# Kernel optimization log

Hardware: AMD Instinct MI355X
Metric: run time of the kernel (lower is better)

The kernel has to match this reference:

```python
import jax, jax.numpy as jnp
import numpy as np

B, D_IN, H, OUT = 4096, 2048, 4096, 1000
TEMPERATURE = 0.5


def _l2_normalize(w):
    return w / jnp.linalg.norm(w, axis=1, keepdims=True)


def setup_inputs() -> dict:
    key = jax.random.key(0)
    ks = jax.random.split(key, 8)
    x = jax.random.normal(ks[0], (B, D_IN), dtype=jnp.float32)
    kohonen_weights = _l2_normalize(jax.random.normal(ks[1], (H, D_IN), dtype=jnp.float32))
    # MLP: 4096 -> 2048 -> 1024 -> 1000 (hidden_layers=2, div=2)
    def lin(k, fan_in, fan_out):
        kw, kb = jax.random.split(k)
        bound = 1.0 / np.sqrt(fan_in)
        W = jax.random.uniform(kw, (fan_out, fan_in), minval=-bound, maxval=bound, dtype=jnp.float32)
        b = jax.random.uniform(kb, (fan_out,), minval=-bound, maxval=bound, dtype=jnp.float32)
        return W, b
    w1, b1 = lin(ks[2], H, H // 2)
    w2, b2 = lin(ks[3], H // 2, H // 4)
    w3, b3 = lin(ks[4], H // 4, OUT)
    return {"x": x, "kohonen_weights": kohonen_weights,
            "w1": w1, "b1": b1, "w2": w2, "b2": b2, "w3": w3, "b3": b3}


def reference(x, kohonen_weights, w1, b1, w2, b2, w3, b3):
    # pairwise euclidean distances [B, H] via expanded GEMM (cdist p=2)
    x2 = jnp.sum(x * x, axis=1, keepdims=True)            # [B,1]
    w2sq = jnp.sum(kohonen_weights * kohonen_weights, axis=1)  # [H]
    d2 = x2 + w2sq[None, :] - 2.0 * (x @ kohonen_weights.T)
    distances = jnp.sqrt(jnp.maximum(d2, 1e-12))
    winners = jnp.argmin(distances, axis=1)
    soft = jax.nn.softmax(-distances / TEMPERATURE, axis=1)
    # MLP (dropout=0 / eval mode)
    h = jax.nn.relu(soft @ w1.T + b1)
    h = jax.nn.relu(h @ w2.T + b2)
    output = h @ w3.T + b3
    return output, winners
```

## Files before the change

### kernel.cpp

```cpp
#include <hip/hip_runtime.h>
#include <hip/hip_bf16.h>
#include <stdint.h>

typedef __attribute__((ext_vector_type(4))) float f32x4;
typedef __attribute__((ext_vector_type(8))) __bf16 bf16x8;
typedef unsigned short u16;
typedef unsigned long long u64;

__device__ __forceinline__ u16 f2bf(float f){
  unsigned u = __float_as_uint(f);
  u += 0x7fffu + ((u >> 16) & 1u);
  return (u16)(u >> 16);
}
__device__ __forceinline__ float bf2f(u16 v){
  return __uint_as_float(((unsigned)v) << 16);
}

__device__ __forceinline__ void gload16(const u16* g, u16* l){
  __builtin_amdgcn_global_load_lds(
      (__attribute__((address_space(1))) void*)g,
      (__attribute__((address_space(3))) void*)l, 16, 0, 0);
}

template<int N> __device__ __forceinline__ void waitcnt_vm(){
  if constexpr (N==0) asm volatile("s_waitcnt vmcnt(0)" ::: "memory");
  else if constexpr (N==4) asm volatile("s_waitcnt vmcnt(4)" ::: "memory");
  else if constexpr (N==8) asm volatile("s_waitcnt vmcnt(8)" ::: "memory");
}

__global__ __launch_bounds__(64)
void cvt_rows(const float* __restrict__ src, u16* __restrict__ dst,
              float* __restrict__ sq)
{
#pragma clang fp contract(off)
  const int row = blockIdx.x;
  const int l = threadIdx.x;
  const float* r = src + (size_t)row * 2048;
  const f32x4* r4 = (const f32x4*)r;
  ushort4* d4 = (ushort4*)(dst + (size_t)row * 2048);
#pragma unroll
  for (int i = 0; i < 8; i++){
    f32x4 v = r4[l + 64*i];
    ushort4 o;
    o.x = f2bf(v.x); o.y = f2bf(v.y); o.z = f2bf(v.z); o.w = f2bf(v.w);
    d4[l + 64*i] = o;
  }
  float leaf = 0.f;
  if (l < 16){
    const f32x4* p4 = (const f32x4*)(r + l*128);
    f32x4 a0 = {0.f,0.f,0.f,0.f}, a1 = {0.f,0.f,0.f,0.f};
#pragma unroll
    for (int i = 0; i < 32; i += 2){
      f32x4 v0 = p4[i], v1 = p4[i+1];
      a0 = a0 + v0*v0;
      a1 = a1 + v1*v1;
    }
    leaf = ((a0.x+a0.y)+(a0.z+a0.w))+((a1.x+a1.y)+(a1.z+a1.w));
  }
#pragma unroll
  for (int s = 1; s < 16; s <<= 1){
    float o = __shfl_down(leaf, s);
    if ((l & (2*s - 1)) == 0) leaf = leaf + o;
  }
  if (l == 0) sq[row] = leaf;
}

__global__ __launch_bounds__(256)
void cvt_mat(const float* __restrict__ src, u16* __restrict__ dst, int n4)
{
  const f32x4* s4 = (const f32x4*)src;
  ushort4* d4 = (ushort4*)dst;
  for (int i = blockIdx.x*256 + threadIdx.x; i < n4; i += gridDim.x*256){
    f32x4 v = s4[i];
    ushort4 o;
    o.x = f2bf(v.x); o.y = f2bf(v.y); o.z = f2bf(v.z); o.w = f2bf(v.w);
    d4[i] = o;
  }
}

__global__ __launch_bounds__(512, 2)
void gemm8p(const u16* __restrict__ A, int lda,
            const u16* __restrict__ Bm, int ldb,
            u16* __restrict__ Cb, int N, int Kpp, int nbn, int blkpp)
{
  constexpr int BUFB = 65536;
  extern __shared__ char lds[];
  const int t = threadIdx.x;
  const int nwg = gridDim.x;
  const int cpx = nwg >> 3;
  const int bid = blockIdx.x;
  const int wg  = (bid & 7)*cpx + (bid >> 3);
  const int piece = wg / blkpp;
  const int rem = wg % blkpp;
  const int bm = rem / nbn, bn = rem % nbn;
  const int brow = bm*256, bcol = bn*256;
  const u16* Ab = A + (size_t)brow*lda + (size_t)piece*Kpp;
  const u16* Bb = Bm + (size_t)bcol*ldb + (size_t)piece*Kpp;
  u16* Cp = Cb + (size_t)piece * 4096 * N;

  const int l = t & 63, w = t >> 6;
  const int wm = w >> 2, wn = w & 3;
  const int wr = wm*128, wc = wn*64;
  const int fr = l & 15, fq = l >> 4;
  const int cb0 = (fq ^ (fr & 7)) << 4;
  const int cb1 = ((4 + fq) ^ (fr & 7)) << 4;
  const int scol8 = ((t & 7) ^ ((t >> 3) & 7)) * 8;
  const int srow = t >> 3;

  const int nt = Kpp >> 6;
  f32x4 acc[8][4] = {};

  auto stage_half = [&](int kt, int h){
    const int nb = kt & 1;
    const u16* src = (h < 2) ? Ab : Bb;
    const int ld = (h < 2) ? lda : ldb;
    const u16* s0 = src + (size_t)((h & 1)*128 + srow)*ld + kt*64 + scol8;
    char* d = lds + nb*BUFB + (h >> 1)*32768 + (h & 1)*16384 + t*16;
    gload16(s0, (u16*)d);
    gload16(s0 + (size_t)64*ld, (u16*)(d + 8192));
  };
  auto ldA = [&](int buf, int m, int cb)->bf16x8 {
    return *(const bf16x8*)(lds + buf*BUFB + (wr + m*16 + fr)*128 + cb);
  };
  auto ldB = [&](int buf, int n, int cb)->bf16x8 {
    return *(const bf16x8*)(lds + buf*BUFB + 32768 + (wc + n*16 + fr)*128 + cb);
  };

  stage_half(0,0); stage_half(0,1); stage_half(0,2); stage_half(0,3);
  stage_half(1,0); stage_half(1,1);
  waitcnt_vm<4>();
  __builtin_amdgcn_s_barrier();

  for (int kt = 0; kt < nt; kt++){
    const int buf = kt & 1;
    bf16x8 av0[8], av1[8], bv0[4], bv1[4];

#pragma unroll
    for (int m = 0; m < 8; m++) av0[m] = ldA(buf, m, cb0);
#pragma unroll
    for (int n = 0; n < 4; n++) bv0[n] = ldB(buf, n, cb0);
    if (kt + 1 < nt) stage_half(kt + 1, 2);
    __builtin_amdgcn_s_setprio(1);
#pragma unroll
    for (int m = 0; m < 8; m++)
#pragma unroll
      for (int n = 0; n < 4; n++)
        acc[m][n] = __builtin_amdgcn_mfma_f32_16x16x32_bf16(av0[m], bv0[n], acc[m][n], 0, 0, 0);
    __builtin_amdgcn_s_setprio(0);
#pragma unroll
    for (int m = 0; m < 8; m++) av1[m] = ldA(buf, m, cb1);
    if (kt + 1 < nt) stage_half(kt + 1, 3);
    asm volatile("s_waitcnt lgkmcnt(0)" ::: "memory");
    __builtin_amdgcn_s_barrier();

#pragma unroll
    for (int n = 0; n < 4; n++) bv1[n] = ldB(buf, n, cb1);
    if (kt + 2 < nt) stage_half(kt + 2, 0);
    __builtin_amdgcn_s_setprio(1);
#pragma unroll
    for (int m = 0; m < 4; m++)
#pragma unroll
      for (int n = 0; n < 4; n++)
        acc[m][n] = __builtin_amdgcn_mfma_f32_16x16x32_bf16(av1[m], bv1[n], acc[m][n], 0, 0, 0);
    __builtin_amdgcn_s_setprio(0);
    if (kt + 2 < nt) stage_half(kt + 2, 1);
    __builtin_amdgcn_s_setprio(1);
#pragma unroll
    for (int m = 4; m < 8; m++)
#pragma unroll
      for (int n = 0; n < 4; n++)
        acc[m][n] = __builtin_amdgcn_mfma_f32_16x16x32_bf16(av1[m], bv1[n], acc[m][n], 0, 0, 0);
    __builtin_amdgcn_s_setprio(0);

    if (kt + 1 < nt){
      if (kt <= nt - 3) waitcnt_vm<4>();
      else              waitcnt_vm<0>();
      __builtin_amdgcn_s_barrier();
    }
  }

  __builtin_amdgcn_s_barrier();
  u16* ep = (u16*)(lds + w*16384);
#pragma unroll
  for (int m = 0; m < 8; m++)
#pragma unroll
    for (int n = 0; n < 4; n++)
#pragma unroll
      for (int r = 0; r < 4; r++)
        ep[(m*16 + fq*4 + r)*64 + n*16 + fr] = f2bf(acc[m][n][r]);
  asm volatile("s_waitcnt lgkmcnt(0)" ::: "memory");
  const int erow = l >> 3, ecb = (l & 7)*16;
#pragma unroll
  for (int it = 0; it < 16; it++){
    const int row = it*8 + erow;
    f32x4 v = *(const f32x4*)((const char*)ep + row*128 + ecb);
    char* gp = (char*)Cp + (((size_t)(brow + wr + row))*N + (bcol + wc))*2 + ecb;
    *(f32x4*)gp = v;
  }
}

__global__ __launch_bounds__(256)
void combine_relu(const u16* __restrict__ p0, const u16* __restrict__ p1,
                  const float* __restrict__ bias, u16* __restrict__ out)
{
  const int n4 = 4096*2048/4;
  for (int i = blockIdx.x*256 + threadIdx.x; i < n4; i += gridDim.x*256){
    ushort4 a = ((const ushort4*)p0)[i];
    ushort4 b = ((const ushort4*)p1)[i];
    const int col = (i*4) & 2047;
    f32x4 bi = *(const f32x4*)(bias + col);
    ushort4 o;
    o.x = f2bf(fmaxf(bf2f(a.x) + bf2f(b.x) + bi.x, 0.f));
    o.y = f2bf(fmaxf(bf2f(a.y) + bf2f(b.y) + bi.y, 0.f));
    o.z = f2bf(fmaxf(bf2f(a.z) + bf2f(b.z) + bi.z, 0.f));
    o.w = f2bf(fmaxf(bf2f(a.w) + bf2f(b.w) + bi.w, 0.f));
    ((ushort4*)out)[i] = o;
  }
}

template<int BM, int BN, int WM, int WN, int EPI, int MINW>
__global__ __launch_bounds__(WM*WN*64, MINW)
void gemm_p(const u16* __restrict__ A, const u16* __restrict__ Bm,
            float* __restrict__ Cf, u16* __restrict__ Cb,
            const float* __restrict__ bias,
            int M, int N, int K, int ncols, int nbn)
{
  constexpr int T  = WM*WN*64;
  constexpr int FM = BM/(WM*16);
  constexpr int FN = BN/(WN*16);
  constexpr int ABYTES = BM*64;
  constexpr int BUFB   = (BM+BN)*64;
  constexpr int RA = ABYTES/(T*16);
  constexpr int RB = (BN*64)/(T*16);
  constexpr int IF = RA + RB;
  extern __shared__ char lds[];

  const int t = threadIdx.x;
  const int nwg = gridDim.x;
  const int cpx = nwg >> 3;
  const int bid = blockIdx.x;
  const int wg  = (bid & 7)*cpx + (bid >> 3);
  const int bm = wg / nbn, bn = wg % nbn;
  const int brow = bm*BM, bcol = bn*BN;

  const int l = t & 63, w = t >> 6;
  const int wm = w / WN, wn = w % WN;
  const int wr = wm*(FM*16), wc = wn*(FN*16);
  const int fr = l & 15, fq = l >> 4, fk = fq*8;
  const int xk = fk ^ (((fr >> 1) & 3) << 3);

  const int srow = t >> 2;
  const int scol = ((t & 3)*8) ^ (((t >> 3) & 3) << 3);

  const u16* agp[RA]; const u16* bgp[RB];
#pragma unroll
  for (int r = 0; r < RA; r++)
    agp[r] = A + (size_t)(brow + r*(T>>2) + srow)*K + scol;
#pragma unroll
  for (int r = 0; r < RB; r++)
    bgp[r] = Bm + (size_t)(bcol + r*(T>>2) + srow)*K + scol;

  f32x4 acc[FM][FN] = {};
  const int nt = K >> 5;

  auto stageA = [&](int kt, int buf){
    char* dst = lds + buf*BUFB + t*16;
#pragma unroll
    for (int r = 0; r < RA; r++)
      gload16(agp[r] + (kt << 5), (u16*)(dst + r*T*16));
  };
  auto stageB = [&](int kt, int buf){
    char* dst = lds + buf*BUFB + ABYTES + t*16;
#pragma unroll
    for (int r = 0; r < RB; r++)
      gload16(bgp[r] + (kt << 5), (u16*)(dst + r*T*16));
  };

  stageA(0, 0); stageB(0, 0);
  stageA(1, 1); stageB(1, 1);
  stageA(2, 2); stageB(2, 2);
  waitcnt_vm<8>();
  __builtin_amdgcn_s_barrier();

  for (int kt = 0; kt < nt; kt++){
    const int buf = kt & 3;
    const u16* As = (const u16*)(lds + buf*BUFB);
    const u16* Bs = (const u16*)(lds + buf*BUFB + ABYTES);
    const bool pre = (kt + 3 < nt);
    const int nbuf = (kt + 3) & 3;

    bf16x8 av[FM], bv[FN];
#pragma unroll
    for (int m = 0; m < FM; m++)
      av[m] = *(const bf16x8*)(As + (wr + m*16 + fr)*32 + xk);
#pragma unroll
    for (int n = 0; n < FN; n++)
      bv[n] = *(const bf16x8*)(Bs + (wc + n*16 + fr)*32 + xk);
    if (pre){ stageA(kt + 3, nbuf); stageB(kt + 3, nbuf); }
    __builtin_amdgcn_s_setprio(1);
#pragma unroll
    for (int m = 0; m < FM; m++)
#pragma unroll
      for (int n = 0; n < FN; n++)
        acc[m][n] = __builtin_amdgcn_mfma_f32_16x16x32_bf16(av[m], bv[n], acc[m][n], 0, 0, 0);
    __builtin_amdgcn_s_setprio(0);

    if (kt + 1 < nt){
      if (kt + 3 < nt)      waitcnt_vm<8>();
      else if (kt + 2 < nt) waitcnt_vm<4>();
      else                  waitcnt_vm<0>();
      __builtin_amdgcn_s_barrier();
    }
  }

  __builtin_amdgcn_s_barrier();
  if (EPI == 1){
    u16* ep = (u16*)(lds + w*8192);
#pragma unroll
    for (int n = 0; n < FN; n++){
      const float bvv = bias[bcol + wc + n*16 + fr];
#pragma unroll
      for (int m = 0; m < FM; m++)
#pragma unroll
        for (int r = 0; r < 4; r++)
          ep[(m*16 + fq*4 + r)*64 + n*16 + fr] = f2bf(fmaxf(acc[m][n][r] + bvv, 0.f));
    }
    asm volatile("s_waitcnt lgkmcnt(0)" ::: "memory");
    const int erow = l >> 3, ecb = (l & 7)*16;
#pragma unroll
    for (int it = 0; it < 8; it++){
      const int row = it*8 + erow;
      f32x4 v = *(const f32x4*)((const char*)ep + row*128 + ecb);
      char* gp = (char*)Cb + (((size_t)(brow + wr + row))*N + (bcol + wc))*2 + ecb;
      *(f32x4*)gp = v;
    }
  } else {
    float* ep = (float*)(lds + w*16384);
#pragma unroll
    for (int n = 0; n < FN; n++){
      const int gcol = bcol + wc + n*16 + fr;
      const float bvv = (gcol < ncols) ? bias[gcol] : 0.f;
#pragma unroll
      for (int m = 0; m < FM; m++)
#pragma unroll
        for (int r = 0; r < 4; r++)
          ep[(m*16 + fq*4 + r)*64 + n*16 + fr] = acc[m][n][r] + bvv;
    }
    asm volatile("s_waitcnt lgkmcnt(0)" ::: "memory");
    const int erow = l >> 4, ecb = (l & 15)*16;
    const int gcol0 = bcol + wc + (l & 15)*4;
#pragma unroll
    for (int it = 0; it < 16; it++){
      const int row = it*4 + erow;
      f32x4 v = *(const f32x4*)((const char*)ep + row*256 + ecb);
      if (gcol0 < ncols)
        *(f32x4*)(Cf + (size_t)(brow + wr + row)*ncols + gcol0) = v;
    }
  }
}

__global__ __launch_bounds__(256)
void row_softmax(const u16* __restrict__ Sb, const float* __restrict__ x2,
                 const float* __restrict__ w2sq,
                 const float* __restrict__ x, const float* __restrict__ W,
                 u16* __restrict__ soft, float* __restrict__ winners)
{
  const int b = blockIdx.x, t = threadIdx.x;
  const float x2b = x2[b];
  const ushort4* S4 = (const ushort4*)(Sb + (size_t)b*4096);
  const f32x4* W24 = (const f32x4*)w2sq;
  float dv[16];
  float bd = 3.0e38f; int bc = 0;
#pragma unroll
  for (int i = 0; i < 4; i++){
    ushort4 s = S4[t + 256*i];
    f32x4 wv = W24[t + 256*i];
    float sf[4] = {bf2f(s.x), bf2f(s.y), bf2f(s.z), bf2f(s.w)};
#pragma unroll
    for (int j = 0; j < 4; j++){
      float u = x2b + wv[j];
      float d2 = u - 2.0f*sf[j];
      float d = __fsqrt_rn(fmaxf(d2, 1e-12f));
      dv[i*4 + j] = d;
      if (d < bd){ bd = d; bc = (t + 256*i)*4 + j; }
    }
  }
  u64 key = ((u64)__float_as_uint(bd) << 32) | (unsigned)bc;
#pragma unroll
  for (int s = 1; s < 64; s <<= 1){
    u64 o = __shfl_xor(key, s);
    if (o < key) key = o;
  }
  __shared__ u64 wk[4];
  __shared__ double csum[4];
  __shared__ float fred[4];
  __shared__ int ccnt;
  __shared__ int cand[32];
  if ((t & 63) == 0) wk[t >> 6] = key;
  if (t == 0) ccnt = 0;
  __syncthreads();
  u64 k0 = wk[0];
  if (wk[1] < k0) k0 = wk[1];
  if (wk[2] < k0) k0 = wk[2];
  if (wk[3] < k0) k0 = wk[3];
  const float dmin = __uint_as_float((unsigned)(k0 >> 32));

  const float thr = dmin + 0.01f;
#pragma unroll
  for (int i = 0; i < 4; i++)
#pragma unroll
    for (int j = 0; j < 4; j++)
      if (dv[i*4 + j] <= thr){
        int p = atomicAdd(&ccnt, 1);
        if (p < 32) cand[p] = (t + 256*i)*4 + j;
      }
  __syncthreads();
  const int nc = min(ccnt, 32);

  float bestd = 3.0e38f; int besti = 0x7fffffff;
  const f32x4* xp = (const f32x4*)(x + (size_t)b*2048) + t*2;
  f32x4 xv0 = xp[0], xv1 = xp[1];
  for (int c = 0; c < nc; c++){
    const int h = cand[c];
    const f32x4* wp = (const f32x4*)(W + (size_t)h*2048) + t*2;
    f32x4 wv0 = wp[0], wv1 = wp[1];
    double a = 0.0;
#pragma unroll
    for (int j = 0; j < 4; j++) a += (double)xv0[j]*(double)wv0[j];
#pragma unroll
    for (int j = 0; j < 4; j++) a += (double)xv1[j]*(double)wv1[j];
#pragma unroll
    for (int s = 1; s < 64; s <<= 1) a += __shfl_xor(a, s);
    if ((t & 63) == 0) csum[t >> 6] = a;
    __syncthreads();
    if (t == 0){
      double tt = (csum[0] + csum[1]) + (csum[2] + csum[3]);
      float t32 = (float)tt;
      float u = x2b + w2sq[h];
      float d2 = u - 2.0f*t32;
      float d = __fsqrt_rn(fmaxf(d2, 1e-12f));
      if (d < bestd || (d == bestd && h < besti)){ bestd = d; besti = h; }
    }
    __syncthreads();
  }
  if (t == 0) winners[b] = (float)besti;

  float es = 0.f;
#pragma unroll
  for (int i = 0; i < 16; i++) es += __expf(-2.0f*(dv[i] - dmin));
#pragma unroll
  for (int s = 1; s < 64; s <<= 1) es += __shfl_xor(es, s);
  if ((t & 63) == 0) fred[t >> 6] = es;
  __syncthreads();
  const float tot = (fred[0] + fred[1]) + (fred[2] + fred[3]);
  const float inv = 1.0f / tot;
  ushort4* o4 = (ushort4*)(soft + (size_t)b*4096);
#pragma unroll
  for (int i = 0; i < 4; i++){
    ushort4 o;
    o.x = f2bf(__expf(-2.0f*(dv[i*4+0] - dmin))*inv);
    o.y = f2bf(__expf(-2.0f*(dv[i*4+1] - dmin))*inv);
    o.z = f2bf(__expf(-2.0f*(dv[i*4+2] - dmin))*inv);
    o.w = f2bf(__expf(-2.0f*(dv[i*4+3] - dmin))*inv);
    o4[t + 256*i] = o;
  }
}

extern "C" void kernel_launch(void* const* d_in, const int* in_sizes, int n_in,
                              void* d_out, int out_size, void* d_ws, size_t ws_size,
                              hipStream_t stream)
{
  const float* x  = (const float*)d_in[0];
  const float* Wk = (const float*)d_in[1];
  const float* w1 = (const float*)d_in[2];
  const float* b1 = (const float*)d_in[3];
  const float* w2 = (const float*)d_in[4];
  const float* b2 = (const float*)d_in[5];
  const float* w3 = (const float*)d_in[6];
  const float* b3 = (const float*)d_in[7];
  float* out = (float*)d_out;
  float* winners = out + (size_t)4096*1000;

  char* ws = (char*)d_ws;
  const size_t MB = 1u << 20;
  u16* Sb    = (u16*)(ws);
  u16* soft  = (u16*)(ws + 32*MB);
  u16* w1b   = (u16*)(ws + 64*MB);
  u16* w2b   = (u16*)(ws + 80*MB);
  u16* w3b   = (u16*)(ws + 84*MB);
  float* x2  = (float*)(ws + 86*MB);
  float* w2s = x2 + 4096;
  u16* xb    = (u16*)(ws + 88*MB);
  u16* wb    = (u16*)(ws + 104*MB);
  u16* P0    = (u16*)(ws + 88*MB);
  u16* P1    = (u16*)(ws + 104*MB);
  u16* h1    = (u16*)(ws);
  u16* h2    = (u16*)(ws + 16*MB);

  cvt_rows<<<4096, 64, 0, stream>>>(x, xb, x2);
  cvt_rows<<<4096, 64, 0, stream>>>(Wk, wb, w2s);
  cvt_mat<<<2048, 256, 0, stream>>>(w1, w1b, 2048*4096/4);
  cvt_mat<<<1024, 256, 0, stream>>>(w2, w2b, 1024*2048/4);
  hipMemsetAsync(w3b, 0, (size_t)1024*1024*2, stream);
  cvt_mat<<<512, 256, 0, stream>>>(w3, w3b, 1000*1024/4);

  hipFuncSetAttribute((const void*)gemm8p,
                      hipFuncAttributeMaxDynamicSharedMemorySize, 131072);

  gemm8p<<<256, 512, 131072, stream>>>(xb, 2048, wb, 2048, Sb,
                                       4096, 2048, 16, 256);

  row_softmax<<<4096, 256, 0, stream>>>(Sb, x2, w2s, x, Wk, soft, winners);

  gemm8p<<<256, 512, 131072, stream>>>(soft, 4096, w1b, 4096, P0,
                                       2048, 2048, 8, 128);
  combine_relu<<<2048, 256, 0, stream>>>(P0, P1, b1, h1);

  hipFuncSetAttribute((const void*)gemm_p<128,128,2,2,1,3>,
                      hipFuncAttributeMaxDynamicSharedMemorySize, 4*256*64);
  gemm_p<128,128,2,2,1,3><<<256, 256, 4*256*64, stream>>>(
      h1, w2b, nullptr, h2, b2, 4096, 1024, 2048, 0, 8);

  hipFuncSetAttribute((const void*)gemm_p<128,128,2,2,2,3>,
                      hipFuncAttributeMaxDynamicSharedMemorySize, 4*256*64);
  gemm_p<128,128,2,2,2,3><<<256, 256, 4*256*64, stream>>>(
      h2, w3b, out, nullptr, b3, 4096, 1024, 1024, 1000, 8);
}
```

Baseline: 259.1 us.

## Replace 256x256 GEMM with 256x128 tile, 3-stage K-32 pipeline

Swaps the 512-thread, 256x256-tile, double-buffered K=64 GEMM for a 256-thread kernel using 256x128 tiles and a triple-buffered K=32 LDS pipeline with a simpler single-phase loop. The grid doubles to 512 workgroups and LDS drops to 72KB, with an epilogue row padding added to cut bank conflicts. The aim is more workgroups per CU and deeper prefetch to hide global-load latency. The cost is more barriers per unit of K and less reuse per tile, since the B panel is narrower and each K step is shorter.

Result: slower. 282.8 us (+9.1%).

```diff
diff --git a/kernel.cpp b/kernel.cpp
--- a/kernel.cpp
+++ b/kernel.cpp
@@ -23,9 +23,11 @@
 }
 
 template<int N> __device__ __forceinline__ void waitcnt_vm(){
-  if constexpr (N==0) asm volatile("s_waitcnt vmcnt(0)" ::: "memory");
-  else if constexpr (N==4) asm volatile("s_waitcnt vmcnt(4)" ::: "memory");
-  else if constexpr (N==8) asm volatile("s_waitcnt vmcnt(8)" ::: "memory");
+  if constexpr (N==0)  asm volatile("s_waitcnt vmcnt(0)" ::: "memory");
+  else if constexpr (N==4)  asm volatile("s_waitcnt vmcnt(4)" ::: "memory");
+  else if constexpr (N==6)  asm volatile("s_waitcnt vmcnt(6)" ::: "memory");
+  else if constexpr (N==8)  asm volatile("s_waitcnt vmcnt(8)" ::: "memory");
+  else if constexpr (N==12) asm volatile("s_waitcnt vmcnt(12)" ::: "memory");
 }
 
 __global__ __launch_bounds__(64)
@@ -78,12 +80,13 @@
   }
 }
 
-__global__ __launch_bounds__(512, 2)
-void gemm8p(const u16* __restrict__ A, int lda,
-            const u16* __restrict__ Bm, int ldb,
-            u16* __restrict__ Cb, int N, int Kpp, int nbn, int blkpp)
-{
-  constexpr int BUFB = 65536;
+__global__ __launch_bounds__(256, 2)
+void gemmA(const u16* __restrict__ A, int lda,
+           const u16* __restrict__ Bm, int ldb,
+           u16* __restrict__ Cb, int N, int Kpp, int nbn, int blkpp)
+{
+  constexpr int BUFB = 24576;
+  constexpr int ABYTES = 16384;
   extern __shared__ char lds[];
   const int t = threadIdx.x;
   const int nwg = gridDim.x;
@@ -93,107 +96,90 @@
   const int piece = wg / blkpp;
   const int rem = wg % blkpp;
   const int bm = rem / nbn, bn = rem % nbn;
-  const int brow = bm*256, bcol = bn*256;
+  const int brow = bm*256, bcol = bn*128;
   const u16* Ab = A + (size_t)brow*lda + (size_t)piece*Kpp;
   const u16* Bb = Bm + (size_t)bcol*ldb + (size_t)piece*Kpp;
   u16* Cp = Cb + (size_t)piece * 4096 * N;
 
   const int l = t & 63, w = t >> 6;
-  const int wm = w >> 2, wn = w & 3;
+  const int wm = w >> 1, wn = w & 1;
   const int wr = wm*128, wc = wn*64;
   const int fr = l & 15, fq = l >> 4;
-  const int cb0 = (fq ^ (fr & 7)) << 4;
-  const int cb1 = ((4 + fq) ^ (fr & 7)) << 4;
-  const int scol8 = ((t & 7) ^ ((t >> 3) & 7)) * 8;
-  const int srow = t >> 3;
-
-  const int nt = Kpp >> 6;
+  const int xk = (fq ^ ((fr >> 1) & 3))*8;
+
+  const int srow = t >> 2;
+  const int scol = ((t & 3) ^ ((t >> 3) & 3))*8;
+
+  const u16* agp[4]; const u16* bgp[2];
+#pragma unroll
+  for (int r = 0; r < 4; r++)
+    agp[r] = Ab + (size_t)(r*64 + srow)*lda + scol;
+#pragma unroll
+  for (int r = 0; r < 2; r++)
+    bgp[r] = Bb + (size_t)(r*64 + srow)*ldb + scol;
+
   f32x4 acc[8][4] = {};
-
-  auto stage_half = [&](int kt, int h){
-    const int nb = kt & 1;
-    const u16* src = (h < 2) ? Ab : Bb;
-    const int ld = (h < 2) ? lda : ldb;
-    const u16* s0 = src + (size_t)((h & 1)*128 + srow)*ld + kt*64 + scol8;
-    char* d = lds + nb*BUFB + (h >> 1)*32768 + (h & 1)*16384 + t*16;
-    gload16(s0, (u16*)d);
-    gload16(s0 + (size_t)64*ld, (u16*)(d + 8192));
+  const int nt = Kpp >> 5;
+
+  auto stage = [&](int kt, int buf){
+    char* dst = lds + buf*BUFB + t*16;
+#pragma unroll
+    for (int r = 0; r < 4; r++)
+      gload16(agp[r] + (kt << 5), (u16*)(dst + r*4096));
+#pragma unroll
+    for (int r = 0; r < 2; r++)
+      gload16(bgp[r] + (kt << 5), (u16*)(dst + ABYTES + r*4096));
   };
-  auto ldA = [&](int buf, int m, int cb)->bf16x8 {
-    return *(const bf16x8*)(lds + buf*BUFB + (wr + m*16 + fr)*128 + cb);
-  };
-  auto ldB = [&](int buf, int n, int cb)->bf16x8 {
-    return *(const bf16x8*)(lds + buf*BUFB + 32768 + (wc + n*16 + fr)*128 + cb);
-  };
-
-  stage_half(0,0); stage_half(0,1); stage_half(0,2); stage_half(0,3);
-  stage_half(1,0); stage_half(1,1);
-  waitcnt_vm<4>();
+
+  stage(0, 0); stage(1, 1); stage(2, 2);
+  waitcnt_vm<12>();
   __builtin_amdgcn_s_barrier();
 
+  int buf = 0;
   for (int kt = 0; kt < nt; kt++){
-    const int buf = kt & 1;
-    bf16x8 av0[8], av1[8], bv0[4], bv1[4];
-
-#pragma unroll
-    for (int m = 0; m < 8; m++) av0[m] = ldA(buf, m, cb0);
-#pragma unroll
-    for (int n = 0; n < 4; n++) bv0[n] = ldB(buf, n, cb0);
-    if (kt + 1 < nt) stage_half(kt + 1, 2);
+    const u16* As = (const u16*)(lds + buf*BUFB);
+    const u16* Bs = (const u16*)(lds + buf*BUFB + ABYTES);
+    const int nbuf = (buf + 2 < 3) ? buf + 2 : buf - 1;
+
+    bf16x8 av[8], bv[4];
+#pragma unroll
+    for (int m = 0; m < 8; m++)
+      av[m] = *(const bf16x8*)(As + (wr + m*16 + fr)*32 + xk);
+#pragma unroll
+    for (int n = 0; n < 4; n++)
+      bv[n] = *(const bf16x8*)(Bs + (wc + n*16 + fr)*32 + xk);
+    if (kt + 2 < nt) stage(kt + 2, nbuf);
     __builtin_amdgcn_s_setprio(1);
 #pragma unroll
     for (int m = 0; m < 8; m++)
 #pragma unroll
       for (int n = 0; n < 4; n++)
-        acc[m][n] = __builtin_amdgcn_mfma_f32_16x16x32_bf16(av0[m], bv0[n], acc[m][n], 0, 0, 0);
+        acc[m][n] = __builtin_amdgcn_mfma_f32_16x16x32_bf16(av[m], bv[n], acc[m][n], 0, 0, 0);
     __builtin_amdgcn_s_setprio(0);
-#pragma unroll
-    for (int m = 0; m < 8; m++) av1[m] = ldA(buf, m, cb1);
-    if (kt + 1 < nt) stage_half(kt + 1, 3);
-    asm volatile("s_waitcnt lgkmcnt(0)" ::: "memory");
-    __builtin_amdgcn_s_barrier();
-
-#pragma unroll
-    for (int n = 0; n < 4; n++) bv1[n] = ldB(buf, n, cb1);
-    if (kt + 2 < nt) stage_half(kt + 2, 0);
-    __builtin_amdgcn_s_setprio(1);
-#pragma unroll
-    for (int m = 0; m < 4; m++)
-#pragma unroll
-      for (int n = 0; n < 4; n++)
-        acc[m][n] = __builtin_amdgcn_mfma_f32_16x16x32_bf16(av1[m], bv1[n], acc[m][n], 0, 0, 0);
-    __builtin_amdgcn_s_setprio(0);
-    if (kt + 2 < nt) stage_half(kt + 2, 1);
-    __builtin_amdgcn_s_setprio(1);
-#pragma unroll
-    for (int m = 4; m < 8; m++)
-#pragma unroll
-      for (int n = 0; n < 4; n++)
-        acc[m][n] = __builtin_amdgcn_mfma_f32_16x16x32_bf16(av1[m], bv1[n], acc[m][n], 0, 0, 0);
-    __builtin_amdgcn_s_setprio(0);
 
     if (kt + 1 < nt){
-      if (kt <= nt - 3) waitcnt_vm<4>();
-      else              waitcnt_vm<0>();
+      if (kt + 2 < nt) waitcnt_vm<6>();
+      else             waitcnt_vm<0>();
       __builtin_amdgcn_s_barrier();
     }
+    buf = (buf + 1 < 3) ? buf + 1 : 0;
   }
 
   __builtin_amdgcn_s_barrier();
-  u16* ep = (u16*)(lds + w*16384);
+  u16* ep = (u16*)(lds + w*17408);
 #pragma unroll
   for (int m = 0; m < 8; m++)
 #pragma unroll
     for (int n = 0; n < 4; n++)
 #pragma unroll
       for (int r = 0; r < 4; r++)
-        ep[(m*16 + fq*4 + r)*64 + n*16 + fr] = f2bf(acc[m][n][r]);
+        ep[(m*16 + fq*4 + r)*68 + n*16 + fr] = f2bf(acc[m][n][r]);
   asm volatile("s_waitcnt lgkmcnt(0)" ::: "memory");
   const int erow = l >> 3, ecb = (l & 7)*16;
 #pragma unroll
   for (int it = 0; it < 16; it++){
     const int row = it*8 + erow;
-    f32x4 v = *(const f32x4*)((const char*)ep + row*128 + ecb);
+    f32x4 v = *(const f32x4*)((const char*)ep + row*136 + ecb);
     char* gp = (char*)Cp + (((size_t)(brow + wr + row))*N + (bcol + wc))*2 + ecb;
     *(f32x4*)gp = v;
   }
@@ -232,7 +218,6 @@
   constexpr int BUFB   = (BM+BN)*64;
   constexpr int RA = ABYTES/(T*16);
   constexpr int RB = (BN*64)/(T*16);
-  constexpr int IF = RA + RB;
   extern __shared__ char lds[];
 
   const int t = threadIdx.x;
@@ -504,16 +489,16 @@
   hipMemsetAsync(w3b, 0, (size_t)1024*1024*2, stream);
   cvt_mat<<<512, 256, 0, stream>>>(w3, w3b, 1000*1024/4);
 
-  hipFuncSetAttribute((const void*)gemm8p,
-                      hipFuncAttributeMaxDynamicSharedMemorySize, 131072);
-
-  gemm8p<<<256, 512, 131072, stream>>>(xb, 2048, wb, 2048, Sb,
-                                       4096, 2048, 16, 256);
+  hipFuncSetAttribute((const void*)gemmA,
+                      hipFuncAttributeMaxDynamicSharedMemorySize, 73728);
+
+  gemmA<<<512, 256, 73728, stream>>>(xb, 2048, wb, 2048, Sb,
+                                     4096, 2048, 32, 512);
 
   row_softmax<<<4096, 256, 0, stream>>>(Sb, x2, w2s, x, Wk, soft, winners);
 
-  gemm8p<<<256, 512, 131072, stream>>>(soft, 4096, w1b, 4096, P0,
-                                       2048, 2048, 8, 128);
+  gemmA<<<512, 256, 73728, stream>>>(soft, 4096, w1b, 4096, P0,
+                                     2048, 2048, 16, 256);
   combine_relu<<<2048, 256, 0, stream>>>(P0, P1, b1, h1);
 
   hipFuncSetAttribute((const void*)gemm_p<128,128,2,2,1,3>,
```

## Triple-buffer A tiles in big GEMM and fuse conversion kernels

Applied to the files above, without the earlier changes.

The 256x256 GEMM now uses 160KB of LDS: the A operand gets a three-deep ring buffer and B a double buffer. This removes the mid-iteration barrier and lets A prefetch run two tiles ahead. The epilogue LDS staging rows are padded to 68 elements to cut bank conflicts. The six input-conversion launches and the memset are merged into two kernels, with w3 zero padding done inline. The larger LDS footprint limits occupancy to one workgroup per CU.

New measurement: 251.0 us. 3.1% less time.

```diff
diff --git a/kernel.cpp b/kernel.cpp
--- a/kernel.cpp
+++ b/kernel.cpp
@@ -23,17 +23,22 @@
 }
 
 template<int N> __device__ __forceinline__ void waitcnt_vm(){
-  if constexpr (N==0) asm volatile("s_waitcnt vmcnt(0)" ::: "memory");
-  else if constexpr (N==4) asm volatile("s_waitcnt vmcnt(4)" ::: "memory");
-  else if constexpr (N==8) asm volatile("s_waitcnt vmcnt(8)" ::: "memory");
+  if constexpr (N==0)  asm volatile("s_waitcnt vmcnt(0)" ::: "memory");
+  else if constexpr (N==4)  asm volatile("s_waitcnt vmcnt(4)" ::: "memory");
+  else if constexpr (N==8)  asm volatile("s_waitcnt vmcnt(8)" ::: "memory");
 }
 
 __global__ __launch_bounds__(64)
-void cvt_rows(const float* __restrict__ src, u16* __restrict__ dst,
-              float* __restrict__ sq)
+void cvt_rows2(const float* __restrict__ x, const float* __restrict__ Wk,
+               u16* __restrict__ xb, u16* __restrict__ wb,
+               float* __restrict__ x2, float* __restrict__ w2s)
 {
 #pragma clang fp contract(off)
-  const int row = blockIdx.x;
+  const int bid = blockIdx.x;
+  const int row = bid & 4095;
+  const float* src = (bid < 4096) ? x : Wk;
+  u16* dst = (bid < 4096) ? xb : wb;
+  float* sq = (bid < 4096) ? x2 : w2s;
   const int l = threadIdx.x;
   const float* r = src + (size_t)row * 2048;
   const f32x4* r4 = (const f32x4*)r;
@@ -66,24 +71,41 @@
 }
 
 __global__ __launch_bounds__(256)
-void cvt_mat(const float* __restrict__ src, u16* __restrict__ dst, int n4)
-{
-  const f32x4* s4 = (const f32x4*)src;
-  ushort4* d4 = (ushort4*)dst;
-  for (int i = blockIdx.x*256 + threadIdx.x; i < n4; i += gridDim.x*256){
-    f32x4 v = s4[i];
+void cvt_w(const float* __restrict__ w1, const float* __restrict__ w2,
+           const float* __restrict__ w3,
+           u16* __restrict__ w1b, u16* __restrict__ w2b, u16* __restrict__ w3b)
+{
+  const int N1 = 2097152;
+  const int N2 = N1 + 524288;
+  const int N3 = N2 + 262144;
+  for (int i = blockIdx.x*256 + threadIdx.x; i < N3; i += gridDim.x*256){
+    f32x4 v;
+    ushort4* dp;
+    if (i < N1){
+      v = ((const f32x4*)w1)[i];
+      dp = (ushort4*)w1b + i;
+    } else if (i < N2){
+      v = ((const f32x4*)w2)[i - N1];
+      dp = (ushort4*)w2b + (i - N1);
+    } else {
+      const int j = i - N2;
+      const int row = j >> 8;
+      const int col4 = (j & 255)*4;
+      if (row < 1000) v = *(const f32x4*)(w3 + (size_t)row*1024 + col4);
+      else            v = f32x4{0.f,0.f,0.f,0.f};
+      dp = (ushort4*)w3b + j;
+    }
     ushort4 o;
     o.x = f2bf(v.x); o.y = f2bf(v.y); o.z = f2bf(v.z); o.w = f2bf(v.w);
-    d4[i] = o;
-  }
-}
-
-__global__ __launch_bounds__(512, 2)
-void gemm8p(const u16* __restrict__ A, int lda,
-            const u16* __restrict__ Bm, int ldb,
-            u16* __restrict__ Cb, int N, int Kpp, int nbn, int blkpp)
-{
-  constexpr int BUFB = 65536;
+    *dp = o;
+  }
+}
+
+__global__ __launch_bounds__(512, 1)
+void gemmN(const u16* __restrict__ A, int lda,
+           const u16* __restrict__ Bm, int ldb,
+           u16* __restrict__ Cb, int N, int Kpp, int nbn, int blkpp)
+{
   extern __shared__ char lds[];
   const int t = threadIdx.x;
   const int nwg = gridDim.x;
@@ -110,36 +132,43 @@
   const int nt = Kpp >> 6;
   f32x4 acc[8][4] = {};
 
-  auto stage_half = [&](int kt, int h){
-    const int nb = kt & 1;
-    const u16* src = (h < 2) ? Ab : Bb;
-    const int ld = (h < 2) ? lda : ldb;
-    const u16* s0 = src + (size_t)((h & 1)*128 + srow)*ld + kt*64 + scol8;
-    char* d = lds + nb*BUFB + (h >> 1)*32768 + (h & 1)*16384 + t*16;
-    gload16(s0, (u16*)d);
-    gload16(s0 + (size_t)64*ld, (u16*)(d + 8192));
+  auto stageA = [&](int kt, int buf){
+    const u16* s0 = Ab + (size_t)srow*lda + kt*64 + scol8;
+    char* d = lds + buf*32768 + t*16;
+#pragma unroll
+    for (int r = 0; r < 4; r++)
+      gload16(s0 + (size_t)r*64*lda, (u16*)(d + r*8192));
+  };
+  auto stageB = [&](int kt){
+    const u16* s0 = Bb + (size_t)srow*ldb + kt*64 + scol8;
+    char* d = lds + 98304 + (kt & 1)*32768 + t*16;
+#pragma unroll
+    for (int r = 0; r < 4; r++)
+      gload16(s0 + (size_t)r*64*ldb, (u16*)(d + r*8192));
   };
   auto ldA = [&](int buf, int m, int cb)->bf16x8 {
-    return *(const bf16x8*)(lds + buf*BUFB + (wr + m*16 + fr)*128 + cb);
+    return *(const bf16x8*)(lds + buf*32768 + (wr + m*16 + fr)*128 + cb);
   };
-  auto ldB = [&](int buf, int n, int cb)->bf16x8 {
-    return *(const bf16x8*)(lds + buf*BUFB + 32768 + (wc + n*16 + fr)*128 + cb);
+  auto ldB = [&](int kt, int n, int cb)->bf16x8 {
+    return *(const bf16x8*)(lds + 98304 + (kt & 1)*32768 + (wc + n*16 + fr)*128 + cb);
   };
 
-  stage_half(0,0); stage_half(0,1); stage_half(0,2); stage_half(0,3);
-  stage_half(1,0); stage_half(1,1);
+  stageA(0, 0); stageB(0);
+  __builtin_amdgcn_sched_barrier(0);
+  stageA(1, 1);
   waitcnt_vm<4>();
   __builtin_amdgcn_s_barrier();
 
+  int ra = 0, sa = 2;
   for (int kt = 0; kt < nt; kt++){
-    const int buf = kt & 1;
     bf16x8 av0[8], av1[8], bv0[4], bv1[4];
 
 #pragma unroll
-    for (int m = 0; m < 8; m++) av0[m] = ldA(buf, m, cb0);
-#pragma unroll
-    for (int n = 0; n < 4; n++) bv0[n] = ldB(buf, n, cb0);
-    if (kt + 1 < nt) stage_half(kt + 1, 2);
+    for (int m = 0; m < 8; m++) av0[m] = ldA(ra, m, cb0);
+#pragma unroll
+    for (int n = 0; n < 4; n++) bv0[n] = ldB(kt, n, cb0);
+    if (kt + 1 < nt) stageB(kt + 1);
+    __builtin_amdgcn_sched_barrier(0);
     __builtin_amdgcn_s_setprio(1);
 #pragma unroll
     for (int m = 0; m < 8; m++)
@@ -147,53 +176,44 @@
       for (int n = 0; n < 4; n++)
         acc[m][n] = __builtin_amdgcn_mfma_f32_16x16x32_bf16(av0[m], bv0[n], acc[m][n], 0, 0, 0);
     __builtin_amdgcn_s_setprio(0);
-#pragma unroll
-    for (int m = 0; m < 8; m++) av1[m] = ldA(buf, m, cb1);
-    if (kt + 1 < nt) stage_half(kt + 1, 3);
-    asm volatile("s_waitcnt lgkmcnt(0)" ::: "memory");
-    __builtin_amdgcn_s_barrier();
-
-#pragma unroll
-    for (int n = 0; n < 4; n++) bv1[n] = ldB(buf, n, cb1);
-    if (kt + 2 < nt) stage_half(kt + 2, 0);
+
+#pragma unroll
+    for (int m = 0; m < 8; m++) av1[m] = ldA(ra, m, cb1);
+#pragma unroll
+    for (int n = 0; n < 4; n++) bv1[n] = ldB(kt, n, cb1);
+    if (kt + 2 < nt) stageA(kt + 2, sa);
     __builtin_amdgcn_s_setprio(1);
 #pragma unroll
-    for (int m = 0; m < 4; m++)
+    for (int m = 0; m < 8; m++)
 #pragma unroll
       for (int n = 0; n < 4; n++)
         acc[m][n] = __builtin_amdgcn_mfma_f32_16x16x32_bf16(av1[m], bv1[n], acc[m][n], 0, 0, 0);
     __builtin_amdgcn_s_setprio(0);
-    if (kt + 2 < nt) stage_half(kt + 2, 1);
-    __builtin_amdgcn_s_setprio(1);
-#pragma unroll
-    for (int m = 4; m < 8; m++)
-#pragma unroll
-      for (int n = 0; n < 4; n++)
-        acc[m][n] = __builtin_amdgcn_mfma_f32_16x16x32_bf16(av1[m], bv1[n], acc[m][n], 0, 0, 0);
-    __builtin_amdgcn_s_setprio(0);
 
     if (kt + 1 < nt){
-      if (kt <= nt - 3) waitcnt_vm<4>();
-      else              waitcnt_vm<0>();
+      if (kt + 2 < nt) waitcnt_vm<4>();
+      else             waitcnt_vm<0>();
       __builtin_amdgcn_s_barrier();
     }
+    ra = (ra == 2) ? 0 : ra + 1;
+    sa = (sa == 2) ? 0 : sa + 1;
   }
 
   __builtin_amdgcn_s_barrier();
-  u16* ep = (u16*)(lds + w*16384);
+  u16* ep = (u16*)(lds + w*17408);
 #pragma unroll
   for (int m = 0; m < 8; m++)
 #pragma unroll
     for (int n = 0; n < 4; n++)
 #pragma unroll
       for (int r = 0; r < 4; r++)
-        ep[(m*16 + fq*4 + r)*64 + n*16 + fr] = f2bf(acc[m][n][r]);
+        ep[(m*16 + fq*4 + r)*68 + n*16 + fr] = f2bf(acc[m][n][r]);
   asm volatile("s_waitcnt lgkmcnt(0)" ::: "memory");
   const int erow = l >> 3, ecb = (l & 7)*16;
 #pragma unroll
   for (int it = 0; it < 16; it++){
     const int row = it*8 + erow;
-    f32x4 v = *(const f32x4*)((const char*)ep + row*128 + ecb);
+    f32x4 v = *(const f32x4*)((const char*)ep + row*136 + ecb);
     char* gp = (char*)Cp + (((size_t)(brow + wr + row))*N + (bcol + wc))*2 + ecb;
     *(f32x4*)gp = v;
   }
@@ -232,7 +252,6 @@
   constexpr int BUFB   = (BM+BN)*64;
   constexpr int RA = ABYTES/(T*16);
   constexpr int RB = (BN*64)/(T*16);
-  constexpr int IF = RA + RB;
   extern __shared__ char lds[];
 
   const int t = threadIdx.x;
@@ -497,23 +516,19 @@
   u16* h1    = (u16*)(ws);
   u16* h2    = (u16*)(ws + 16*MB);
 
-  cvt_rows<<<4096, 64, 0, stream>>>(x, xb, x2);
-  cvt_rows<<<4096, 64, 0, stream>>>(Wk, wb, w2s);
-  cvt_mat<<<2048, 256, 0, stream>>>(w1, w1b, 2048*4096/4);
-  cvt_mat<<<1024, 256, 0, stream>>>(w2, w2b, 1024*2048/4);
-  hipMemsetAsync(w3b, 0, (size_t)1024*1024*2, stream);
-  cvt_mat<<<512, 256, 0, stream>>>(w3, w3b, 1000*1024/4);
-
-  hipFuncSetAttribute((const void*)gemm8p,
-                      hipFuncAttributeMaxDynamicSharedMemorySize, 131072);
-
-  gemm8p<<<256, 512, 131072, stream>>>(xb, 2048, wb, 2048, Sb,
-                                       4096, 2048, 16, 256);
+  cvt_rows2<<<8192, 64, 0, stream>>>(x, Wk, xb, wb, x2, w2s);
+  cvt_w<<<2048, 256, 0, stream>>>(w1, w2, w3, w1b, w2b, w3b);
+
+  hipFuncSetAttribute((const void*)gemmN,
+                      hipFuncAttributeMaxDynamicSharedMemorySize, 163840);
+
+  gemmN<<<256, 512, 163840, stream>>>(xb, 2048, wb, 2048, Sb,
+                                      4096, 2048, 16, 256);
 
   row_softmax<<<4096, 256, 0, stream>>>(Sb, x2, w2s, x, Wk, soft, winners);
 
-  gemm8p<<<256, 512, 131072, stream>>>(soft, 4096, w1b, 4096, P0,
-                                       2048, 2048, 8, 128);
+  gemmN<<<256, 512, 163840, stream>>>(soft, 4096, w1b, 4096, P0,
+                                      2048, 2048, 8, 128);
   combine_relu<<<2048, 256, 0, stream>>>(P0, P1, b1, h1);
 
   hipFuncSetAttribute((const void*)gemm_p<128,128,2,2,1,3>,
```
